# Kernel tuning notes

Measured on AMD Instinct MI355X. Metric: run time of the kernel, lower is better.

## Reference

```python
import jax, jax.numpy as jnp
import numpy as np

B, L = 256, 256
TAU = 0.01


def setup_inputs() -> dict:
    key = jax.random.key(0)
    k1, k2, k3, k4 = jax.random.split(key, 4)
    x = jax.random.normal(k1, (B, L, B), dtype=jnp.float32)
    target = jax.random.normal(k2, (B, L, B), dtype=jnp.float32)
    mask = jnp.ones((B, L), dtype=jnp.int32)  # prefix-valid mask per query; all clips valid
    query_labels = jax.random.randint(k3, (B,), 0, B, dtype=jnp.int64)
    label_mat = jax.random.randint(k4, (B, B), 0, 2, dtype=jnp.int32)  # label_dict[i] -> row i
    return {"x": x, "target": target, "mask": mask, "query_labels": query_labels, "label_mat": label_mat}


def reference(x, target, mask, query_labels, label_mat):
    # x, target: [B, L, B] (batch, clips, queries); mask: [B(queries), L]
    xs = jax.nn.softmax(x, axis=1)
    ts = jax.nn.softmax(target, axis=1)
    m = (mask > 0).astype(xs.dtype)  # [i(query), l]
    # mask target clips per query i (equivalent to the original's :m prefix slice
    # because mask is a contiguous prefix of valid clips)
    tsm = ts * m.T[None, :, :]  # [c, l, i]
    # sim[i, b, c] = sum_l xs[b, l, i] * ts[c, l, i] * m[i, l]  (per-query B x B matmul)
    sim = jnp.einsum('bli,cli->ibc', xs, tsm)
    logits = sim / TAU
    # original computes -log(exp(n_ji)/sum_c exp(n_jc)) == -log_softmax over c, picked at class i
    logp = jax.nn.log_softmax(logits, axis=-1)  # [i, j, c]
    per = jnp.diagonal(logp, axis1=0, axis2=2)  # per[j, i] = logp[i, j, i]
    loss = -(label_mat.astype(xs.dtype).T * per).sum() / x.shape[0]
    return loss
```

## Files before the change

### kernel.cpp

```cpp
#include <hip/hip_runtime.h>
#include <hip/hip_bf16.h>

#define NB 256
#define NL 256
#define SCALE 100.0f

typedef __attribute__((ext_vector_type(4))) unsigned int u32x4;
typedef __attribute__((ext_vector_type(8))) __bf16 bfrag8;
typedef __attribute__((ext_vector_type(4))) float f32x4;

static __device__ __forceinline__ unsigned int pack2bf(float a, float b) {
  union { float f; unsigned int u; } ua, ub;
  ua.f = a; ub.f = b;
  unsigned int ra = (ua.u + 0x7FFFu + ((ua.u >> 16) & 1u)) >> 16;
  unsigned int rb = (ub.u + 0x7FFFu + ((ub.u >> 16) & 1u)) & 0xFFFF0000u;
  return ra | rb;
}

__global__ __launch_bounds__(1024, 2) void softmax_t(
    const float* __restrict__ x, const float* __restrict__ tgt,
    unsigned int* __restrict__ xsT, unsigned int* __restrict__ tsT)
{
  const int b = blockIdx.x;
  const bool is_t = (blockIdx.y != 0);
  const int tid = threadIdx.x;
  const int i = tid & 255;
  const int h = tid >> 8;
  const float* src = (is_t ? tgt : x) + (size_t)b * (NL * NB) + i;
  unsigned int* dstb = (is_t ? tsT : xsT);

  __shared__ float s_sum[4][256];
  __shared__ __align__(16) unsigned char stg[256 * 128];

  float s = 0.f;
  #pragma unroll 8
  for (int k = 0; k < 64; ++k) s += __expf(src[(size_t)(h * 64 + k) * NB]);
  s_sum[h][i] = s;
  __syncthreads();
  const float inv = 1.0f / (s_sum[0][i] + s_sum[1][i] + s_sum[2][i] + s_sum[3][i]);

  const int r0 = tid >> 3;
  const int c  = tid & 7;

  for (int lc = 0; lc < 4; ++lc) {
    float v[16];
    #pragma unroll
    for (int k = 0; k < 16; ++k)
      v[k] = __expf(src[(size_t)(lc * 64 + h * 16 + k) * NB]) * inv;
    u32x4 p0, p1;
    p0.x = pack2bf(v[0], v[1]);   p0.y = pack2bf(v[2], v[3]);
    p0.z = pack2bf(v[4], v[5]);   p0.w = pack2bf(v[6], v[7]);
    p1.x = pack2bf(v[8], v[9]);   p1.y = pack2bf(v[10], v[11]);
    p1.z = pack2bf(v[12], v[13]); p1.w = pack2bf(v[14], v[15]);
    *reinterpret_cast<u32x4*>(&stg[i * 128 + (((h * 2 + 0) ^ (i & 7)) << 4)]) = p0;
    *reinterpret_cast<u32x4*>(&stg[i * 128 + (((h * 2 + 1) ^ (i & 7)) << 4)]) = p1;
    __syncthreads();
    u32x4 q0 = *reinterpret_cast<const u32x4*>(&stg[r0 * 128 + ((c ^ (r0 & 7)) << 4)]);
    u32x4 q1 = *reinterpret_cast<const u32x4*>(&stg[(r0 + 128) * 128 + ((c ^ (r0 & 7)) << 4)]);
    *reinterpret_cast<u32x4*>(dstb + ((size_t)r0 * 256 + b) * 128 + lc * 32 + c * 4) = q0;
    *reinterpret_cast<u32x4*>(dstb + ((size_t)(r0 + 128) * 256 + b) * 128 + lc * 32 + c * 4) = q1;
    __syncthreads();
  }
}

__global__ __launch_bounds__(256, 2) void gemm_lse(
    const unsigned short* __restrict__ xsT,
    const unsigned short* __restrict__ tsT,
    const int* __restrict__ mask,
    const int* __restrict__ label_mat,
    float* __restrict__ out)
{
  const int n  = blockIdx.x;
  const int g  = n & 7;
  const int q  = n >> 3;
  const int i  = ((q >> 2) << 3) + g;
  const int jt = q & 3;
  const int t  = threadIdx.x;
  const int w  = t >> 6;
  const int lane = t & 63;

  __shared__ __align__(16) unsigned char As[64 * 128];
  __shared__ __align__(16) unsigned char Bs[256 * 128];
  __shared__ __align__(16) unsigned short s_mask[NL];
  __shared__ float s_rmax[4][64];
  __shared__ float s_rsum[4][64];
  __shared__ float s_diag[64];

  const unsigned short* Ag = xsT + ((size_t)i * NB + jt * 64) * NL;
  const unsigned short* Bg = tsT + (size_t)i * NB * NL;

  const int srow = t >> 3;
  const int sch  = t & 7;

  s_mask[t] = (mask[i * NL + t] > 0) ? (unsigned short)0xFFFFu : (unsigned short)0u;

  f32x4 acc[4][4];
  #pragma unroll
  for (int a = 0; a < 4; ++a)
    #pragma unroll
    for (int cc = 0; cc < 4; ++cc) acc[a][cc] = f32x4{0.f, 0.f, 0.f, 0.f};

  u32x4 areg[2], breg[8];

  #pragma unroll
  for (int r = 0; r < 2; ++r)
    areg[r] = *reinterpret_cast<const u32x4*>(Ag + (size_t)(srow + r * 32) * NL + sch * 8);
  #pragma unroll
  for (int r = 0; r < 8; ++r)
    breg[r] = *reinterpret_cast<const u32x4*>(Bg + (size_t)(srow + r * 32) * NL + sch * 8);

  __syncthreads();

  #pragma unroll
  for (int kc = 0; kc < 4; ++kc) {
    u32x4 mk = *reinterpret_cast<const u32x4*>(&s_mask[kc * 64 + sch * 8]);
    #pragma unroll
    for (int r = 0; r < 2; ++r) {
      int row = srow + r * 32;
      u32x4 a = areg[r];
      a.x &= mk.x; a.y &= mk.y; a.z &= mk.z; a.w &= mk.w;
      *reinterpret_cast<u32x4*>(&As[row * 128 + ((sch ^ (row & 7)) << 4)]) = a;
    }
    #pragma unroll
    for (int r = 0; r < 8; ++r) {
      int row = srow + r * 32;
      *reinterpret_cast<u32x4*>(&Bs[row * 128 + ((sch ^ (row & 7)) << 4)]) = breg[r];
    }
    __syncthreads();
    if (kc < 3) {
      const int kofs = (kc + 1) * 64;
      #pragma unroll
      for (int r = 0; r < 2; ++r)
        areg[r] = *reinterpret_cast<const u32x4*>(Ag + (size_t)(srow + r * 32) * NL + kofs + sch * 8);
      #pragma unroll
      for (int r = 0; r < 8; ++r)
        breg[r] = *reinterpret_cast<const u32x4*>(Bg + (size_t)(srow + r * 32) * NL + kofs + sch * 8);
    }
    #pragma unroll
    for (int kk = 0; kk < 2; ++kk) {
      const int co = kk * 4 + (lane >> 4);
      bfrag8 af[4], bfr[4];
      #pragma unroll
      for (int jf = 0; jf < 4; ++jf) {
        int row = jf * 16 + (lane & 15);
        af[jf] = *reinterpret_cast<const bfrag8*>(&As[row * 128 + ((co ^ (row & 7)) << 4)]);
      }
      #pragma unroll
      for (int cf = 0; cf < 4; ++cf) {
        int row = w * 64 + cf * 16 + (lane & 15);
        bfr[cf] = *reinterpret_cast<const bfrag8*>(&Bs[row * 128 + ((co ^ (row & 7)) << 4)]);
      }
      #pragma unroll
      for (int jf = 0; jf < 4; ++jf)
        #pragma unroll
        for (int cf = 0; cf < 4; ++cf)
          acc[jf][cf] = __builtin_amdgcn_mfma_f32_16x16x32_bf16(
              af[jf], bfr[cf], acc[jf][cf], 0, 0, 0);
    }
    __syncthreads();
  }

  #pragma unroll
  for (int jf = 0; jf < 4; ++jf)
    #pragma unroll
    for (int cf = 0; cf < 4; ++cf) acc[jf][cf] *= SCALE;

  const int rg = (lane >> 4) << 2;

  #pragma unroll
  for (int jf = 0; jf < 4; ++jf) {
    #pragma unroll
    for (int reg = 0; reg < 4; ++reg) {
      float m = fmaxf(fmaxf(acc[jf][0][reg], acc[jf][1][reg]),
                      fmaxf(acc[jf][2][reg], acc[jf][3][reg]));
      #pragma unroll
      for (int off = 1; off < 16; off <<= 1) m = fmaxf(m, __shfl_xor(m, off, 64));
      if ((lane & 15) == 0) s_rmax[w][jf * 16 + rg + reg] = m;
    }
  }
  if (w == (i >> 6) && (lane & 15) == (i & 15)) {
    const int cfd = (i >> 4) & 3;
    #pragma unroll
    for (int jf = 0; jf < 4; ++jf) {
      #pragma unroll
      for (int reg = 0; reg < 4; ++reg) {
        float v = acc[jf][0][reg];
        #pragma unroll
        for (int cf = 1; cf < 4; ++cf)
          v = (cfd == cf) ? acc[jf][cf][reg] : v;
        s_diag[jf * 16 + rg + reg] = v;
      }
    }
  }
  __syncthreads();

  #pragma unroll
  for (int jf = 0; jf < 4; ++jf) {
    #pragma unroll
    for (int reg = 0; reg < 4; ++reg) {
      int row = jf * 16 + rg + reg;
      float gm = fmaxf(fmaxf(s_rmax[0][row], s_rmax[1][row]),
                       fmaxf(s_rmax[2][row], s_rmax[3][row]));
      float sE = 0.f;
      #pragma unroll
      for (int cf = 0; cf < 4; ++cf) sE += __expf(acc[jf][cf][reg] - gm);
      #pragma unroll
      for (int off = 1; off < 16; off <<= 1) sE += __shfl_xor(sE, off, 64);
      if ((lane & 15) == 0) s_rsum[w][row] = sE;
    }
  }
  __syncthreads();

  float contrib = 0.f;
  if (t < 64) {
    const int row = t;
    float gm = fmaxf(fmaxf(s_rmax[0][row], s_rmax[1][row]),
                     fmaxf(s_rmax[2][row], s_rmax[3][row]));
    float tot = s_rsum[0][row] + s_rsum[1][row] + s_rsum[2][row] + s_rsum[3][row];
    float lse = __logf(tot) + gm;
    float lbl = (float)label_mat[i * NB + jt * 64 + row];
    contrib = lbl * (s_diag[row] - lse);
  }
  #pragma unroll
  for (int off = 32; off >= 1; off >>= 1) contrib += __shfl_down(contrib, off, 64);
  if (t == 0) atomicAdd(out, contrib * (-1.0f / 256.0f));
}

extern "C" void kernel_launch(void* const* d_in, const int* in_sizes, int n_in,
                              void* d_out, int out_size, void* d_ws, size_t ws_size,
                              hipStream_t stream) {
  const float* x   = (const float*)d_in[0];
  const float* tgt = (const float*)d_in[1];
  const int* mask  = (const int*)d_in[2];
  const int* label_mat = (const int*)d_in[4];
  float* out = (float*)d_out;

  unsigned int* xsT = (unsigned int*)d_ws;
  unsigned int* tsT = xsT + (size_t)NB * NB * NL / 2;

  hipMemsetAsync(out, 0, sizeof(float), stream);
  softmax_t<<<dim3(NB, 2), 1024, 0, stream>>>(x, tgt, xsT, tsT);
  gemm_lse<<<dim3(1024), 256, 0, stream>>>((const unsigned short*)xsT,
                                           (const unsigned short*)tsT,
                                           mask, label_mat, out);
}
```

Before: 91.82 us.

## Defer softmax normalization into GEMM epilogue using MFMA row/column sums

The first kernel now stores only exp(x) and exp(target) in bf16, dropping the separate pass that read each input once more to compute the softmax denominators. The GEMM kernel recovers those denominators with extra MFMAs against a ones fragment and rescales the accumulators by their reciprocals in the epilogue. The mask is now applied to the A fragments in registers, so the denominators still sum over all clips. This removes a full extra read of both large inputs, at the cost of about 50% more MFMA work. It also risks overflow because exp is taken without subtracting the max, and the denominators are now summed from bf16-rounded values.

```diff
diff --git a/kernel.cpp b/kernel.cpp
--- a/kernel.cpp
+++ b/kernel.cpp
@@ -8,6 +8,8 @@
 typedef __attribute__((ext_vector_type(4))) unsigned int u32x4;
 typedef __attribute__((ext_vector_type(8))) __bf16 bfrag8;
 typedef __attribute__((ext_vector_type(4))) float f32x4;
+
+union BU { bfrag8 f; u32x4 u; };
 
 static __device__ __forceinline__ unsigned int pack2bf(float a, float b) {
   union { float f; unsigned int u; } ua, ub;
@@ -17,7 +19,7 @@
   return ra | rb;
 }
 
-__global__ __launch_bounds__(1024, 2) void softmax_t(
+__global__ __launch_bounds__(1024, 2) void exp_t(
     const float* __restrict__ x, const float* __restrict__ tgt,
     unsigned int* __restrict__ xsT, unsigned int* __restrict__ tsT)
 {
@@ -29,15 +31,7 @@
   const float* src = (is_t ? tgt : x) + (size_t)b * (NL * NB) + i;
   unsigned int* dstb = (is_t ? tsT : xsT);
 
-  __shared__ float s_sum[4][256];
   __shared__ __align__(16) unsigned char stg[256 * 128];
-
-  float s = 0.f;
-  #pragma unroll 8
-  for (int k = 0; k < 64; ++k) s += __expf(src[(size_t)(h * 64 + k) * NB]);
-  s_sum[h][i] = s;
-  __syncthreads();
-  const float inv = 1.0f / (s_sum[0][i] + s_sum[1][i] + s_sum[2][i] + s_sum[3][i]);
 
   const int r0 = tid >> 3;
   const int c  = tid & 7;
@@ -46,7 +40,7 @@
     float v[16];
     #pragma unroll
     for (int k = 0; k < 16; ++k)
-      v[k] = __expf(src[(size_t)(lc * 64 + h * 16 + k) * NB]) * inv;
+      v[k] = __expf(src[(size_t)(lc * 64 + h * 16 + k) * NB]);
     u32x4 p0, p1;
     p0.x = pack2bf(v[0], v[1]);   p0.y = pack2bf(v[2], v[3]);
     p0.z = pack2bf(v[4], v[5]);   p0.w = pack2bf(v[6], v[7]);
@@ -94,11 +88,18 @@
 
   s_mask[t] = (mask[i * NL + t] > 0) ? (unsigned short)0xFFFFu : (unsigned short)0u;
 
-  f32x4 acc[4][4];
-  #pragma unroll
-  for (int a = 0; a < 4; ++a)
+  BU onesbu;
+  onesbu.u = u32x4{0x3F803F80u, 0x3F803F80u, 0x3F803F80u, 0x3F803F80u};
+  const bfrag8 ones = onesbu.f;
+
+  f32x4 acc[4][4], acc_as[4], acc_bs[4];
+  #pragma unroll
+  for (int a = 0; a < 4; ++a) {
+    acc_as[a] = f32x4{0.f, 0.f, 0.f, 0.f};
+    acc_bs[a] = f32x4{0.f, 0.f, 0.f, 0.f};
     #pragma unroll
     for (int cc = 0; cc < 4; ++cc) acc[a][cc] = f32x4{0.f, 0.f, 0.f, 0.f};
+  }
 
   u32x4 areg[2], breg[8];
 
@@ -113,13 +114,10 @@
 
   #pragma unroll
   for (int kc = 0; kc < 4; ++kc) {
-    u32x4 mk = *reinterpret_cast<const u32x4*>(&s_mask[kc * 64 + sch * 8]);
     #pragma unroll
     for (int r = 0; r < 2; ++r) {
       int row = srow + r * 32;
-      u32x4 a = areg[r];
-      a.x &= mk.x; a.y &= mk.y; a.z &= mk.z; a.w &= mk.w;
-      *reinterpret_cast<u32x4*>(&As[row * 128 + ((sch ^ (row & 7)) << 4)]) = a;
+      *reinterpret_cast<u32x4*>(&As[row * 128 + ((sch ^ (row & 7)) << 4)]) = areg[r];
     }
     #pragma unroll
     for (int r = 0; r < 8; ++r) {
@@ -150,20 +148,43 @@
         int row = w * 64 + cf * 16 + (lane & 15);
         bfr[cf] = *reinterpret_cast<const bfrag8*>(&Bs[row * 128 + ((co ^ (row & 7)) << 4)]);
       }
-      #pragma unroll
-      for (int jf = 0; jf < 4; ++jf)
+      u32x4 mk = *reinterpret_cast<const u32x4*>(
+          &s_mask[kc * 64 + kk * 32 + ((lane >> 4) << 3)]);
+      #pragma unroll
+      for (int jf = 0; jf < 4; ++jf) {
+        BU am; am.f = af[jf]; am.u &= mk;
         #pragma unroll
         for (int cf = 0; cf < 4; ++cf)
           acc[jf][cf] = __builtin_amdgcn_mfma_f32_16x16x32_bf16(
-              af[jf], bfr[cf], acc[jf][cf], 0, 0, 0);
-    }
-    __syncthreads();
-  }
-
+              am.f, bfr[cf], acc[jf][cf], 0, 0, 0);
+        acc_as[jf] = __builtin_amdgcn_mfma_f32_16x16x32_bf16(
+            af[jf], ones, acc_as[jf], 0, 0, 0);
+      }
+      #pragma unroll
+      for (int cf = 0; cf < 4; ++cf)
+        acc_bs[cf] = __builtin_amdgcn_mfma_f32_16x16x32_bf16(
+            ones, bfr[cf], acc_bs[cf], 0, 0, 0);
+    }
+    __syncthreads();
+  }
+
+  float ixv[4][4];
   #pragma unroll
   for (int jf = 0; jf < 4; ++jf)
     #pragma unroll
-    for (int cf = 0; cf < 4; ++cf) acc[jf][cf] *= SCALE;
+    for (int reg = 0; reg < 4; ++reg)
+      ixv[jf][reg] = __builtin_amdgcn_rcpf(acc_as[jf][reg]) * SCALE;
+  float itv[4];
+  #pragma unroll
+  for (int cf = 0; cf < 4; ++cf)
+    itv[cf] = __builtin_amdgcn_rcpf(acc_bs[cf][0]);
+  #pragma unroll
+  for (int jf = 0; jf < 4; ++jf)
+    #pragma unroll
+    for (int cf = 0; cf < 4; ++cf)
+      #pragma unroll
+      for (int reg = 0; reg < 4; ++reg)
+        acc[jf][cf][reg] *= ixv[jf][reg] * itv[cf];
 
   const int rg = (lane >> 4) << 2;
 
@@ -239,7 +260,7 @@
   unsigned int* tsT = xsT + (size_t)NB * NB * NL / 2;
 
   hipMemsetAsync(out, 0, sizeof(float), stream);
-  softmax_t<<<dim3(NB, 2), 1024, 0, stream>>>(x, tgt, xsT, tsT);
+  exp_t<<<dim3(NB, 2), 1024, 0, stream>>>(x, tgt, xsT, tsT);
   gemm_lse<<<dim3(1024), 256, 0, stream>>>((const unsigned short*)xsT,
                                            (const unsigned short*)tsT,
                                            mask, label_mat, out);
```

After: 75.98 us. 1.21x faster.

## Defer softmax normalization into GEMM epilogue and read input once

Applied to the files above, without the earlier changes.

The first kernel now stores unnormalized exp values and per-column sums, which removes the separate pass over the input that only computed the softmax denominators. The GEMM applies the reciprocal sums as row and column scales on the accumulator, since the softmax normalization factors out of the per-query matmul. The mask is applied in the exp kernel instead of during the GEMM's shared-memory staging. The intermediate layout is also transposed so the exp kernel's writes are contiguous per batch, at the cost of strided reads in the GEMM. bf16 rounding of unnormalized exps could change precision slightly.

```diff
diff --git a/kernel.cpp b/kernel.cpp
--- a/kernel.cpp
+++ b/kernel.cpp
@@ -6,6 +6,7 @@
 #define SCALE 100.0f
 
 typedef __attribute__((ext_vector_type(4))) unsigned int u32x4;
+typedef __attribute__((ext_vector_type(4))) int i32x4;
 typedef __attribute__((ext_vector_type(8))) __bf16 bfrag8;
 typedef __attribute__((ext_vector_type(4))) float f32x4;
 
@@ -17,9 +18,11 @@
   return ra | rb;
 }
 
-__global__ __launch_bounds__(1024, 2) void softmax_t(
+__global__ __launch_bounds__(1024, 2) void exp_t(
     const float* __restrict__ x, const float* __restrict__ tgt,
-    unsigned int* __restrict__ xsT, unsigned int* __restrict__ tsT)
+    unsigned int* __restrict__ xsT, unsigned int* __restrict__ tsT,
+    const int* __restrict__ mask,
+    float* __restrict__ sumx, float* __restrict__ sumt)
 {
   const int b = blockIdx.x;
   const bool is_t = (blockIdx.y != 0);
@@ -29,24 +32,32 @@
   const float* src = (is_t ? tgt : x) + (size_t)b * (NL * NB) + i;
   unsigned int* dstb = (is_t ? tsT : xsT);
 
+  __shared__ __align__(16) unsigned char stg[256 * 128];
   __shared__ float s_sum[4][256];
-  __shared__ __align__(16) unsigned char stg[256 * 128];
-
-  float s = 0.f;
-  #pragma unroll 8
-  for (int k = 0; k < 64; ++k) s += __expf(src[(size_t)(h * 64 + k) * NB]);
-  s_sum[h][i] = s;
-  __syncthreads();
-  const float inv = 1.0f / (s_sum[0][i] + s_sum[1][i] + s_sum[2][i] + s_sum[3][i]);
 
   const int r0 = tid >> 3;
   const int c  = tid & 7;
 
+  float tsum = 0.f;
+
   for (int lc = 0; lc < 4; ++lc) {
     float v[16];
     #pragma unroll
     for (int k = 0; k < 16; ++k)
-      v[k] = __expf(src[(size_t)(lc * 64 + h * 16 + k) * NB]) * inv;
+      v[k] = __expf(src[(size_t)(lc * 64 + h * 16 + k) * NB]);
+    #pragma unroll
+    for (int k = 0; k < 16; ++k) tsum += v[k];
+    if (is_t) {
+      const i32x4* mrow = reinterpret_cast<const i32x4*>(mask + i * NL + lc * 64 + h * 16);
+      #pragma unroll
+      for (int mq = 0; mq < 4; ++mq) {
+        i32x4 m = mrow[mq];
+        if (m.x <= 0) v[mq * 4 + 0] = 0.f;
+        if (m.y <= 0) v[mq * 4 + 1] = 0.f;
+        if (m.z <= 0) v[mq * 4 + 2] = 0.f;
+        if (m.w <= 0) v[mq * 4 + 3] = 0.f;
+      }
+    }
     u32x4 p0, p1;
     p0.x = pack2bf(v[0], v[1]);   p0.y = pack2bf(v[2], v[3]);
     p0.z = pack2bf(v[4], v[5]);   p0.w = pack2bf(v[6], v[7]);
@@ -56,17 +67,25 @@
     *reinterpret_cast<u32x4*>(&stg[i * 128 + (((h * 2 + 1) ^ (i & 7)) << 4)]) = p1;
     __syncthreads();
     u32x4 q0 = *reinterpret_cast<const u32x4*>(&stg[r0 * 128 + ((c ^ (r0 & 7)) << 4)]);
-    u32x4 q1 = *reinterpret_cast<const u32x4*>(&stg[(r0 + 128) * 128 + ((c ^ (r0 & 7)) << 4)]);
-    *reinterpret_cast<u32x4*>(dstb + ((size_t)r0 * 256 + b) * 128 + lc * 32 + c * 4) = q0;
-    *reinterpret_cast<u32x4*>(dstb + ((size_t)(r0 + 128) * 256 + b) * 128 + lc * 32 + c * 4) = q1;
-    __syncthreads();
+    u32x4 q1 = *reinterpret_cast<const u32x4*>(&stg[(r0 + 128) * 128 + ((c ^ ((r0 + 128) & 7)) << 4)]);
+    *reinterpret_cast<u32x4*>(dstb + ((size_t)b * 256 + r0) * 128 + lc * 32 + c * 4) = q0;
+    *reinterpret_cast<u32x4*>(dstb + ((size_t)b * 256 + r0 + 128) * 128 + lc * 32 + c * 4) = q1;
+    __syncthreads();
+  }
+
+  s_sum[h][i] = tsum;
+  __syncthreads();
+  if (h == 0) {
+    float* so = is_t ? sumt : sumx;
+    so[(size_t)b * 256 + i] = s_sum[0][i] + s_sum[1][i] + s_sum[2][i] + s_sum[3][i];
   }
 }
 
 __global__ __launch_bounds__(256, 2) void gemm_lse(
     const unsigned short* __restrict__ xsT,
     const unsigned short* __restrict__ tsT,
-    const int* __restrict__ mask,
+    const float* __restrict__ sumx,
+    const float* __restrict__ sumt,
     const int* __restrict__ label_mat,
     float* __restrict__ out)
 {
@@ -81,18 +100,18 @@
 
   __shared__ __align__(16) unsigned char As[64 * 128];
   __shared__ __align__(16) unsigned char Bs[256 * 128];
-  __shared__ __align__(16) unsigned short s_mask[NL];
+  __shared__ float s_irx[64];
+  __shared__ float s_ict[256];
   __shared__ float s_rmax[4][64];
   __shared__ float s_rsum[4][64];
   __shared__ float s_diag[64];
 
-  const unsigned short* Ag = xsT + ((size_t)i * NB + jt * 64) * NL;
-  const unsigned short* Bg = tsT + (size_t)i * NB * NL;
-
   const int srow = t >> 3;
   const int sch  = t & 7;
 
-  s_mask[t] = (mask[i * NL + t] > 0) ? (unsigned short)0xFFFFu : (unsigned short)0u;
+  s_ict[t] = __builtin_amdgcn_rcpf(sumt[(size_t)t * 256 + i]);
+  if (t < 64)
+    s_irx[t] = SCALE * __builtin_amdgcn_rcpf(sumx[(size_t)(jt * 64 + t) * 256 + i]);
 
   f32x4 acc[4][4];
   #pragma unroll
@@ -102,40 +121,40 @@
 
   u32x4 areg[2], breg[8];
 
-  #pragma unroll
-  for (int r = 0; r < 2; ++r)
-    areg[r] = *reinterpret_cast<const u32x4*>(Ag + (size_t)(srow + r * 32) * NL + sch * 8);
-  #pragma unroll
-  for (int r = 0; r < 8; ++r)
-    breg[r] = *reinterpret_cast<const u32x4*>(Bg + (size_t)(srow + r * 32) * NL + sch * 8);
-
-  __syncthreads();
-
+  auto load_chunk = [&](int kc) {
+    const int kofs = kc * 64;
+    #pragma unroll
+    for (int r = 0; r < 2; ++r) {
+      int row = srow + r * 32;
+      areg[r] = *reinterpret_cast<const u32x4*>(
+          xsT + ((size_t)(jt * 64 + row) * 256 + i) * 256 + kofs + sch * 8);
+    }
+    #pragma unroll
+    for (int r = 0; r < 8; ++r) {
+      int row = srow + r * 32;
+      breg[r] = *reinterpret_cast<const u32x4*>(
+          tsT + ((size_t)row * 256 + i) * 256 + kofs + sch * 8);
+    }
+  };
+  auto store_chunk = [&]() {
+    #pragma unroll
+    for (int r = 0; r < 2; ++r) {
+      int row = srow + r * 32;
+      *reinterpret_cast<u32x4*>(&As[row * 128 + ((sch ^ (row & 7)) << 4)]) = areg[r];
+    }
+    #pragma unroll
+    for (int r = 0; r < 8; ++r) {
+      int row = srow + r * 32;
+      *reinterpret_cast<u32x4*>(&Bs[row * 128 + ((sch ^ (row & 7)) << 4)]) = breg[r];
+    }
+  };
+
+  load_chunk(0);
   #pragma unroll
   for (int kc = 0; kc < 4; ++kc) {
-    u32x4 mk = *reinterpret_cast<const u32x4*>(&s_mask[kc * 64 + sch * 8]);
-    #pragma unroll
-    for (int r = 0; r < 2; ++r) {
-      int row = srow + r * 32;
-      u32x4 a = areg[r];
-      a.x &= mk.x; a.y &= mk.y; a.z &= mk.z; a.w &= mk.w;
-      *reinterpret_cast<u32x4*>(&As[row * 128 + ((sch ^ (row & 7)) << 4)]) = a;
-    }
-    #pragma unroll
-    for (int r = 0; r < 8; ++r) {
-      int row = srow + r * 32;
-      *reinterpret_cast<u32x4*>(&Bs[row * 128 + ((sch ^ (row & 7)) << 4)]) = breg[r];
-    }
-    __syncthreads();
-    if (kc < 3) {
-      const int kofs = (kc + 1) * 64;
-      #pragma unroll
-      for (int r = 0; r < 2; ++r)
-        areg[r] = *reinterpret_cast<const u32x4*>(Ag + (size_t)(srow + r * 32) * NL + kofs + sch * 8);
-      #pragma unroll
-      for (int r = 0; r < 8; ++r)
-        breg[r] = *reinterpret_cast<const u32x4*>(Bg + (size_t)(srow + r * 32) * NL + kofs + sch * 8);
-    }
+    store_chunk();
+    __syncthreads();
+    if (kc < 3) load_chunk(kc + 1);
     #pragma unroll
     for (int kk = 0; kk < 2; ++kk) {
       const int co = kk * 4 + (lane >> 4);
@@ -143,12 +162,14 @@
       #pragma unroll
       for (int jf = 0; jf < 4; ++jf) {
         int row = jf * 16 + (lane & 15);
-        af[jf] = *reinterpret_cast<const bfrag8*>(&As[row * 128 + ((co ^ (row & 7)) << 4)]);
+        af[jf] = *reinterpret_cast<const bfrag8*>(
+            &As[row * 128 + ((co ^ (row & 7)) << 4)]);
       }
       #pragma unroll
       for (int cf = 0; cf < 4; ++cf) {
         int row = w * 64 + cf * 16 + (lane & 15);
-        bfr[cf] = *reinterpret_cast<const bfrag8*>(&Bs[row * 128 + ((co ^ (row & 7)) << 4)]);
+        bfr[cf] = *reinterpret_cast<const bfrag8*>(
+            &Bs[row * 128 + ((co ^ (row & 7)) << 4)]);
       }
       #pragma unroll
       for (int jf = 0; jf < 4; ++jf)
@@ -160,12 +181,24 @@
     __syncthreads();
   }
 
+  const int rg = (lane >> 4) << 2;
+
+  float fr[4][4], fc[4];
   #pragma unroll
   for (int jf = 0; jf < 4; ++jf)
     #pragma unroll
-    for (int cf = 0; cf < 4; ++cf) acc[jf][cf] *= SCALE;
-
-  const int rg = (lane >> 4) << 2;
+    for (int reg = 0; reg < 4; ++reg)
+      fr[jf][reg] = s_irx[jf * 16 + rg + reg];
+  #pragma unroll
+  for (int cf = 0; cf < 4; ++cf)
+    fc[cf] = s_ict[w * 64 + cf * 16 + (lane & 15)];
+  #pragma unroll
+  for (int jf = 0; jf < 4; ++jf)
+    #pragma unroll
+    for (int cf = 0; cf < 4; ++cf)
+      #pragma unroll
+      for (int reg = 0; reg < 4; ++reg)
+        acc[jf][cf][reg] *= fr[jf][reg] * fc[cf];
 
   #pragma unroll
   for (int jf = 0; jf < 4; ++jf) {
@@ -237,10 +270,12 @@
 
   unsigned int* xsT = (unsigned int*)d_ws;
   unsigned int* tsT = xsT + (size_t)NB * NB * NL / 2;
+  float* sumx = (float*)(tsT + (size_t)NB * NB * NL / 2);
+  float* sumt = sumx + (size_t)NB * NB;
 
   hipMemsetAsync(out, 0, sizeof(float), stream);
-  softmax_t<<<dim3(NB, 2), 1024, 0, stream>>>(x, tgt, xsT, tsT);
+  exp_t<<<dim3(NB, 2), 1024, 0, stream>>>(x, tgt, xsT, tsT, mask, sumx, sumt);
   gemm_lse<<<dim3(1024), 256, 0, stream>>>((const unsigned short*)xsT,
                                            (const unsigned short*)tsT,
-                                           mask, label_mat, out);
-}
+                                           sumx, sumt, label_mat, out);
+}
```

After: 80.69 us. -12.1%, faster.
